# Kernel optimization log

Measured on AMD Instinct MI355X. Metric: run time of the kernel, lower is better.

## Reference

```python
import jax, jax.numpy as jnp
import numpy as np

EMB = 384
GROUPS = 4
B, T = 32, 1024
MAX_DUR = 8
SILENCE_VAL = -11.5129251


def setup_inputs() -> dict:
    key = jax.random.key(0)
    k1, k2, k3, k4, k5 = jax.random.split(key, 5)
    phoneme = jax.random.normal(k1, (B, T, EMB), dtype=jnp.float32)
    durations = jax.random.randint(k2, (B, T + 1), 0, MAX_DUR, dtype=jnp.int32)
    t_out = int(np.asarray(jnp.sum(durations, axis=-1)).max())
    silence_token = jnp.full((EMB,), SILENCE_VAL, dtype=jnp.float32)
    # DurationPredictor params (grouped conv -> ReLU -> 1x1 conv to scalar)
    conv1_w = jax.random.normal(k3, (EMB, EMB // GROUPS, 3), dtype=jnp.float32) * 0.05
    conv1_b = jnp.zeros((EMB,), dtype=jnp.float32)
    conv2_w = jax.random.normal(k4, (1, EMB, 1), dtype=jnp.float32) * 0.05
    conv2_b = jnp.zeros((1,), dtype=jnp.float32)
    return {
        "phoneme": phoneme,
        "silence_token": silence_token,
        "conv1_w": conv1_w,
        "conv1_b": conv1_b,
        "conv2_w": conv2_w,
        "conv2_b": conv2_b,
        "durations": durations,
        "t_out": t_out,
    }


def _duration_predictor(x, conv1_w, conv1_b, conv2_w, conv2_b):
    # x: [B, Tp, E] -> durations_pred [B, Tp]
    xc = jnp.transpose(x, (0, 2, 1))  # [B, E, Tp]
    h = jax.lax.conv_general_dilated(
        xc, conv1_w, window_strides=(1,), padding=((1, 1),),
        dimension_numbers=("NCH", "OIH", "NCH"), feature_group_count=GROUPS)
    h = jax.nn.relu(h + conv1_b[None, :, None])
    d = jax.lax.conv_general_dilated(
        h, conv2_w, window_strides=(1,), padding=((0, 0),),
        dimension_numbers=("NCH", "OIH", "NCH"))
    return d[:, 0, :] + conv2_b[0]  # [B, Tp]


def _regulate(phoneme, durations, t_out):
    # Equivalent to the one-hot mask matmul: frame t gets token j where
    # cumsum[j-1] <= t < cumsum[j]; frames past total length are zero.
    cum = jnp.cumsum(durations, axis=-1)  # [B, Tp]
    pos = jnp.arange(t_out, dtype=cum.dtype)  # [t_out]
    idx = jax.vmap(lambda c: jnp.searchsorted(c, pos, side="right"))(cum)  # [B, t_out]
    valid = pos[None, :] < cum[:, -1:]
    idx = jnp.clip(idx, 0, phoneme.shape[1] - 1)
    gathered = jnp.take_along_axis(phoneme, idx[..., None], axis=1)  # [B, t_out, E]
    return jnp.where(valid[..., None], gathered, jnp.zeros((), phoneme.dtype))


def reference(phoneme, silence_token, conv1_w, conv1_b, conv2_w, conv2_b, durations, t_out):
    Bn = phoneme.shape[0]
    silence = jnp.broadcast_to(silence_token[None, None, :], (Bn, 1, phoneme.shape[2]))
    ph = jnp.concatenate((phoneme, silence), axis=1)  # [B, T+1, E]
    durations_pred = _duration_predictor(ph, conv1_w, conv1_b, conv2_w, conv2_b)
    expanded = _regulate(ph, durations, t_out)  # [B, t_out, E]
    return expanded, durations_pred
```

## Files before the change

### kernel.cpp

```cpp
#include <hip/hip_runtime.h>

#define BATCH 32
#define T_IN 1024
#define TP 1025
#define EMB 384
#define GROUPS 4
#define GC 96
#define KDIM 288

typedef __attribute__((ext_vector_type(8))) short short8;
typedef __attribute__((ext_vector_type(4))) float f32x4;

#define N_WPACK (GROUPS * 9 * 6 * 64 * 8)

__device__ __forceinline__ unsigned short f2bf(float f) {
    union { float f; unsigned u; } v; v.f = f;
    unsigned u = v.u + 0x7fffu + ((v.u >> 16) & 1u);
    return (unsigned short)(u >> 16);
}

__global__ __launch_bounds__(256) void prep_kernel(const float* __restrict__ w1,
                                                   const float* __restrict__ b2,
                                                   unsigned short* __restrict__ wpack,
                                                   float* __restrict__ pred) {
    int i = blockIdx.x * 256 + threadIdx.x;
    if (i < N_WPACK) {
        int j = i & 7;
        int lane = (i >> 3) & 63;
        int rest = i >> 9;
        int nt = rest % 6; rest /= 6;
        int ks = rest % 9;
        int g = rest / 9;
        int oc = nt * 16 + (lane & 15);
        int kk = ks * 32 + (lane >> 4) * 8 + j;
        int k = kk / 96, ic = kk % 96;
        float v = w1[((size_t)(g * GC + oc) * GC + ic) * 3 + k];
        wpack[i] = f2bf(v);
    }
    if (i < BATCH * TP) pred[i] = b2[0];
}

__global__ __launch_bounds__(64) void scan_kernel(const int* __restrict__ dur,
                                                  int* __restrict__ cum) {
    const int b = blockIdx.x;
    const int l = threadIdx.x;
    const int* d = dur + b * TP;
    int* c = cum + b * TP;
    int offset = 0;
    for (int r = 0; r < 17; ++r) {
        int idx = r * 64 + l;
        int v = (idx < TP) ? d[idx] : 0;
        int s = v;
#pragma unroll
        for (int off = 1; off < 64; off <<= 1) {
            int n = __shfl_up(s, off, 64);
            if (l >= off) s += n;
        }
        if (idx < TP) c[idx] = s + offset;
        offset += __shfl(s, 63, 64);
    }
}

__global__ __launch_bounds__(256) void conv_mfma_kernel(const float* __restrict__ phoneme,
                                                        const float* __restrict__ silence,
                                                        const float* __restrict__ b1,
                                                        const float* __restrict__ w2,
                                                        const unsigned short* __restrict__ wpack,
                                                        float* __restrict__ pred) {
    const int tile = blockIdx.x;
    const int g = blockIdx.y;
    const int b = blockIdx.z;
    const int t0 = tile * 64;

    __shared__ __align__(16) unsigned short xs[66][104];
    __shared__ float red[4][16][17];

    const int tid = threadIdx.x;

    for (int e = tid; e < 66 * 24; e += 256) {
        int row = e / 24;
        int v = e - row * 24;
        int r = t0 - 1 + row;
        float4 val;
        if (r < 0 || r > T_IN) {
            val = make_float4(0.f, 0.f, 0.f, 0.f);
        } else if (r == T_IN) {
            val = *(const float4*)(silence + g * GC + v * 4);
        } else {
            val = *(const float4*)(phoneme + ((size_t)(b * T_IN + r)) * EMB + g * GC + v * 4);
        }
        ushort4 pk;
        pk.x = f2bf(val.x); pk.y = f2bf(val.y); pk.z = f2bf(val.z); pk.w = f2bf(val.w);
        *(ushort4*)&xs[row][v * 4] = pk;
    }
    __syncthreads();

    const int w = tid >> 6;
    const int lane = tid & 63;
    const int quad = lane >> 4;
    const int lr = lane & 15;

    f32x4 acc[6];
#pragma unroll
    for (int nt = 0; nt < 6; ++nt) acc[nt] = (f32x4){0.f, 0.f, 0.f, 0.f};

    const unsigned short* wg = wpack + (size_t)g * 9 * 6 * 512;

#pragma unroll
    for (int ks = 0; ks < 9; ++ks) {
        const int k = ks / 3;
        const int icoff = 32 * (ks % 3) + quad * 8;
        const int lrow = w * 16 + lr + k;
        short8 a = *(const short8*)&xs[lrow][icoff];
#pragma unroll
        for (int nt = 0; nt < 6; ++nt) {
            short8 bf = *(const short8*)(wg + ((size_t)(ks * 6 + nt) * 64 + lane) * 8);
            acc[nt] = __builtin_amdgcn_mfma_f32_16x16x32_bf16(a, bf, acc[nt], 0, 0, 0);
        }
    }

    float s[4] = {0.f, 0.f, 0.f, 0.f};
#pragma unroll
    for (int nt = 0; nt < 6; ++nt) {
        int oc = g * GC + nt * 16 + lr;
        float bias = b1[oc];
        float wc = w2[oc];
#pragma unroll
        for (int reg = 0; reg < 4; ++reg) {
            float h = acc[nt][reg] + bias;
            h = h > 0.f ? h : 0.f;
            s[reg] += wc * h;
        }
    }
#pragma unroll
    for (int reg = 0; reg < 4; ++reg) red[w][quad * 4 + reg][lr] = s[reg];
    __syncthreads();

    if (tid < 64) {
        int wv = tid >> 4, m = tid & 15;
        float sum = 0.f;
#pragma unroll
        for (int c2 = 0; c2 < 16; ++c2) sum += red[wv][m][c2];
        int t = t0 + wv * 16 + m;
        if (t < TP) atomicAdd(pred + b * TP + t, sum);
    }
}

__global__ __launch_bounds__(256) void gather_kernel(const float* __restrict__ phoneme,
                                                     const float* __restrict__ silence,
                                                     const int* __restrict__ cum,
                                                     float* __restrict__ out,
                                                     int t_out) {
    const int b = blockIdx.y;
    const int f0 = blockIdx.x * 64;
    const int tid = threadIdx.x;

    __shared__ int sidx[64];
    __shared__ int stotal;

    if (tid == 0) stotal = cum[b * TP + T_IN];
    if (tid < 64) {
        int t = f0 + tid;
        int id = 0;
        if (t < t_out) {
            const int* c = cum + b * TP;
            int lo = 0, hi = TP;
            while (lo < hi) {
                int mid = (lo + hi) >> 1;
                if (c[mid] <= t) lo = mid + 1; else hi = mid;
            }
            id = lo > T_IN ? T_IN : lo;
        }
        sidx[tid] = id;
    }
    __syncthreads();

    const int total = stotal;
    const float4* ph4 = (const float4*)phoneme;
    const float4* s4 = (const float4*)silence;
    float4* out4 = (float4*)out;

    for (int e = tid; e < 64 * 96; e += 256) {
        int fl = e / 96;
        int v = e - fl * 96;
        int t = f0 + fl;
        if (t >= t_out) continue;
        float4 val;
        if (t >= total) {
            val = make_float4(0.f, 0.f, 0.f, 0.f);
        } else {
            int id = sidx[fl];
            val = (id == T_IN) ? s4[v] : ph4[((size_t)(b * T_IN) + id) * 96 + v];
        }
        out4[((size_t)b * t_out + t) * 96 + v] = val;
    }
}

extern "C" void kernel_launch(void* const* d_in, const int* in_sizes, int n_in,
                              void* d_out, int out_size, void* d_ws, size_t ws_size,
                              hipStream_t stream) {
    const float* phoneme = (const float*)d_in[0];
    const float* silence = (const float*)d_in[1];
    const float* conv1_w = (const float*)d_in[2];
    const float* conv1_b = (const float*)d_in[3];
    const float* conv2_w = (const float*)d_in[4];
    const float* conv2_b = (const float*)d_in[5];
    const int* durations = (const int*)d_in[6];
    const int t_out = (out_size - BATCH * TP) / (BATCH * EMB);

    float* out_expanded = (float*)d_out;
    float* out_pred = (float*)d_out + (size_t)BATCH * t_out * EMB;

    int* cum = (int*)d_ws;
    unsigned short* wpack = (unsigned short*)((char*)d_ws + 131200);

    prep_kernel<<<(N_WPACK + 255) / 256, 256, 0, stream>>>(conv1_w, conv2_b, wpack, out_pred);
    scan_kernel<<<BATCH, 64, 0, stream>>>(durations, cum);
    conv_mfma_kernel<<<dim3(17, GROUPS, BATCH), 256, 0, stream>>>(
        phoneme, silence, conv1_b, conv2_w, wpack, out_pred);
    gather_kernel<<<dim3((t_out + 63) / 64, BATCH), 256, 0, stream>>>(
        phoneme, silence, cum, out_expanded, t_out);
}
```

Before: 263.5 us.

## Merge conv groups per block, scatter frame indices, flatten gather

The conv kernel now loads all 384 channels for a 64-frame tile once and assigns one wave per group. Each wave computes four 16-row M tiles, which removes the cross-group atomicAdd and the separate pred initialisation. The duration scan now scatters per-frame token indices (ushort) into workspace in place of the cumulative sums, so the gather kernel skips its per-frame binary search and becomes a flat elementwise copy. The cost is more LDS and accumulator registers per conv block, fewer conv blocks, and serial per-thread scatter loops.

```diff
diff --git a/kernel.cpp b/kernel.cpp
--- a/kernel.cpp
+++ b/kernel.cpp
@@ -6,7 +6,6 @@
 #define EMB 384
 #define GROUPS 4
 #define GC 96
-#define KDIM 288
 
 typedef __attribute__((ext_vector_type(8))) short short8;
 typedef __attribute__((ext_vector_type(4))) float f32x4;
@@ -20,74 +19,83 @@
 }
 
 __global__ __launch_bounds__(256) void prep_kernel(const float* __restrict__ w1,
-                                                   const float* __restrict__ b2,
-                                                   unsigned short* __restrict__ wpack,
-                                                   float* __restrict__ pred) {
+                                                   unsigned short* __restrict__ wpack) {
     int i = blockIdx.x * 256 + threadIdx.x;
-    if (i < N_WPACK) {
-        int j = i & 7;
-        int lane = (i >> 3) & 63;
-        int rest = i >> 9;
-        int nt = rest % 6; rest /= 6;
-        int ks = rest % 9;
-        int g = rest / 9;
-        int oc = nt * 16 + (lane & 15);
-        int kk = ks * 32 + (lane >> 4) * 8 + j;
-        int k = kk / 96, ic = kk % 96;
-        float v = w1[((size_t)(g * GC + oc) * GC + ic) * 3 + k];
-        wpack[i] = f2bf(v);
-    }
-    if (i < BATCH * TP) pred[i] = b2[0];
-}
-
-__global__ __launch_bounds__(64) void scan_kernel(const int* __restrict__ dur,
-                                                  int* __restrict__ cum) {
+    if (i >= N_WPACK) return;
+    int j = i & 7;
+    int lane = (i >> 3) & 63;
+    int rest = i >> 9;
+    int nt = rest % 6; rest /= 6;
+    int ks = rest % 9;
+    int g = rest / 9;
+    int oc = nt * 16 + (lane & 15);
+    int kk = ks * 32 + (lane >> 4) * 8 + j;
+    int k = kk / 96, ic = kk % 96;
+    wpack[i] = f2bf(w1[((size_t)(g * GC + oc) * GC + ic) * 3 + k]);
+}
+
+__global__ __launch_bounds__(256) void scan_scatter_kernel(const int* __restrict__ dur,
+                                                           unsigned short* __restrict__ idx,
+                                                           int t_out) {
     const int b = blockIdx.x;
-    const int l = threadIdx.x;
-    const int* d = dur + b * TP;
-    int* c = cum + b * TP;
-    int offset = 0;
-    for (int r = 0; r < 17; ++r) {
-        int idx = r * 64 + l;
-        int v = (idx < TP) ? d[idx] : 0;
-        int s = v;
-#pragma unroll
-        for (int off = 1; off < 64; off <<= 1) {
-            int n = __shfl_up(s, off, 64);
-            if (l >= off) s += n;
+    const int tid = threadIdx.x;
+    __shared__ int scum[TP];
+
+    if (tid < 64) {
+        const int* d = dur + b * TP;
+        int offset = 0;
+        for (int r = 0; r < 17; ++r) {
+            int i2 = r * 64 + tid;
+            int v = (i2 < TP) ? d[i2] : 0;
+            int s = v;
+#pragma unroll
+            for (int off = 1; off < 64; off <<= 1) {
+                int n = __shfl_up(s, off, 64);
+                if (tid >= off) s += n;
+            }
+            if (i2 < TP) scum[i2] = s + offset;
+            offset += __shfl(s, 63, 64);
         }
-        if (idx < TP) c[idx] = s + offset;
-        offset += __shfl(s, 63, 64);
-    }
+    }
+    __syncthreads();
+
+    unsigned short* ib = idx + (size_t)b * t_out;
+    for (int j = tid; j < TP; j += 256) {
+        int c = scum[j];
+        int d = dur[b * TP + j];
+        for (int f = c - d; f < c; ++f) ib[f] = (unsigned short)j;
+    }
+    const int total = scum[TP - 1];
+    for (int t = total + tid; t < t_out; t += 256) ib[t] = 0xFFFFu;
 }
 
 __global__ __launch_bounds__(256) void conv_mfma_kernel(const float* __restrict__ phoneme,
                                                         const float* __restrict__ silence,
                                                         const float* __restrict__ b1,
                                                         const float* __restrict__ w2,
+                                                        const float* __restrict__ b2,
                                                         const unsigned short* __restrict__ wpack,
                                                         float* __restrict__ pred) {
     const int tile = blockIdx.x;
-    const int g = blockIdx.y;
-    const int b = blockIdx.z;
+    const int b = blockIdx.y;
     const int t0 = tile * 64;
 
-    __shared__ __align__(16) unsigned short xs[66][104];
-    __shared__ float red[4][16][17];
+    __shared__ __align__(16) unsigned short xs[66][392];
+    __shared__ float red[4][64];
 
     const int tid = threadIdx.x;
 
-    for (int e = tid; e < 66 * 24; e += 256) {
-        int row = e / 24;
-        int v = e - row * 24;
+    for (int e = tid; e < 66 * 96; e += 256) {
+        int row = e / 96;
+        int v = e - row * 96;
         int r = t0 - 1 + row;
         float4 val;
         if (r < 0 || r > T_IN) {
             val = make_float4(0.f, 0.f, 0.f, 0.f);
         } else if (r == T_IN) {
-            val = *(const float4*)(silence + g * GC + v * 4);
+            val = *(const float4*)(silence + v * 4);
         } else {
-            val = *(const float4*)(phoneme + ((size_t)(b * T_IN + r)) * EMB + g * GC + v * 4);
+            val = *(const float4*)(phoneme + ((size_t)(b * T_IN + r)) * EMB + v * 4);
         }
         ushort4 pk;
         pk.x = f2bf(val.x); pk.y = f2bf(val.y); pk.z = f2bf(val.z); pk.w = f2bf(val.w);
@@ -95,105 +103,97 @@
     }
     __syncthreads();
 
-    const int w = tid >> 6;
+    const int g = tid >> 6;
     const int lane = tid & 63;
     const int quad = lane >> 4;
     const int lr = lane & 15;
 
-    f32x4 acc[6];
-#pragma unroll
-    for (int nt = 0; nt < 6; ++nt) acc[nt] = (f32x4){0.f, 0.f, 0.f, 0.f};
+    f32x4 acc[4][6];
+#pragma unroll
+    for (int mt = 0; mt < 4; ++mt)
+#pragma unroll
+        for (int nt = 0; nt < 6; ++nt) acc[mt][nt] = (f32x4){0.f, 0.f, 0.f, 0.f};
 
     const unsigned short* wg = wpack + (size_t)g * 9 * 6 * 512;
 
 #pragma unroll
     for (int ks = 0; ks < 9; ++ks) {
-        const int k = ks / 3;
-        const int icoff = 32 * (ks % 3) + quad * 8;
-        const int lrow = w * 16 + lr + k;
-        short8 a = *(const short8*)&xs[lrow][icoff];
+        const int tap = ks / 3;
+        const int col = g * GC + 32 * (ks % 3) + quad * 8;
+        short8 a[4];
+#pragma unroll
+        for (int mt = 0; mt < 4; ++mt)
+            a[mt] = *(const short8*)&xs[mt * 16 + lr + tap][col];
 #pragma unroll
         for (int nt = 0; nt < 6; ++nt) {
             short8 bf = *(const short8*)(wg + ((size_t)(ks * 6 + nt) * 64 + lane) * 8);
-            acc[nt] = __builtin_amdgcn_mfma_f32_16x16x32_bf16(a, bf, acc[nt], 0, 0, 0);
+#pragma unroll
+            for (int mt = 0; mt < 4; ++mt)
+                acc[mt][nt] = __builtin_amdgcn_mfma_f32_16x16x32_bf16(a[mt], bf, acc[mt][nt], 0, 0, 0);
         }
     }
 
-    float s[4] = {0.f, 0.f, 0.f, 0.f};
+    float s[4][4];
+#pragma unroll
+    for (int mt = 0; mt < 4; ++mt)
+#pragma unroll
+        for (int reg = 0; reg < 4; ++reg) s[mt][reg] = 0.f;
 #pragma unroll
     for (int nt = 0; nt < 6; ++nt) {
         int oc = g * GC + nt * 16 + lr;
         float bias = b1[oc];
         float wc = w2[oc];
 #pragma unroll
-        for (int reg = 0; reg < 4; ++reg) {
-            float h = acc[nt][reg] + bias;
-            h = h > 0.f ? h : 0.f;
-            s[reg] += wc * h;
-        }
-    }
-#pragma unroll
-    for (int reg = 0; reg < 4; ++reg) red[w][quad * 4 + reg][lr] = s[reg];
+        for (int mt = 0; mt < 4; ++mt)
+#pragma unroll
+            for (int reg = 0; reg < 4; ++reg) {
+                float h = acc[mt][nt][reg] + bias;
+                h = h > 0.f ? h : 0.f;
+                s[mt][reg] += wc * h;
+            }
+    }
+#pragma unroll
+    for (int off = 1; off < 16; off <<= 1)
+#pragma unroll
+        for (int mt = 0; mt < 4; ++mt)
+#pragma unroll
+            for (int reg = 0; reg < 4; ++reg)
+                s[mt][reg] += __shfl_xor(s[mt][reg], off, 64);
+#pragma unroll
+    for (int mt = 0; mt < 4; ++mt)
+#pragma unroll
+        for (int reg = 0; reg < 4; ++reg)
+            if (lr == mt * 4 + reg) red[g][mt * 16 + quad * 4 + reg] = s[mt][reg];
     __syncthreads();
 
     if (tid < 64) {
-        int wv = tid >> 4, m = tid & 15;
-        float sum = 0.f;
-#pragma unroll
-        for (int c2 = 0; c2 < 16; ++c2) sum += red[wv][m][c2];
-        int t = t0 + wv * 16 + m;
-        if (t < TP) atomicAdd(pred + b * TP + t, sum);
+        int t = t0 + tid;
+        if (t < TP)
+            pred[b * TP + t] = red[0][tid] + red[1][tid] + red[2][tid] + red[3][tid] + b2[0];
     }
 }
 
 __global__ __launch_bounds__(256) void gather_kernel(const float* __restrict__ phoneme,
                                                      const float* __restrict__ silence,
-                                                     const int* __restrict__ cum,
+                                                     const unsigned short* __restrict__ idx,
                                                      float* __restrict__ out,
                                                      int t_out) {
     const int b = blockIdx.y;
-    const int f0 = blockIdx.x * 64;
-    const int tid = threadIdx.x;
-
-    __shared__ int sidx[64];
-    __shared__ int stotal;
-
-    if (tid == 0) stotal = cum[b * TP + T_IN];
-    if (tid < 64) {
-        int t = f0 + tid;
-        int id = 0;
-        if (t < t_out) {
-            const int* c = cum + b * TP;
-            int lo = 0, hi = TP;
-            while (lo < hi) {
-                int mid = (lo + hi) >> 1;
-                if (c[mid] <= t) lo = mid + 1; else hi = mid;
-            }
-            id = lo > T_IN ? T_IN : lo;
-        }
-        sidx[tid] = id;
-    }
-    __syncthreads();
-
-    const int total = stotal;
-    const float4* ph4 = (const float4*)phoneme;
-    const float4* s4 = (const float4*)silence;
-    float4* out4 = (float4*)out;
-
-    for (int e = tid; e < 64 * 96; e += 256) {
-        int fl = e / 96;
-        int v = e - fl * 96;
-        int t = f0 + fl;
-        if (t >= t_out) continue;
-        float4 val;
-        if (t >= total) {
-            val = make_float4(0.f, 0.f, 0.f, 0.f);
-        } else {
-            int id = sidx[fl];
-            val = (id == T_IN) ? s4[v] : ph4[((size_t)(b * T_IN) + id) * 96 + v];
-        }
-        out4[((size_t)b * t_out + t) * 96 + v] = val;
-    }
+    const int nfe = t_out * 96;
+    int e = blockIdx.x * 256 + threadIdx.x;
+    if (e >= nfe) return;
+    int fl = e / 96;
+    int v = e - fl * 96;
+    unsigned short id = idx[(size_t)b * t_out + fl];
+    float4 val;
+    if (id == 0xFFFFu) {
+        val = make_float4(0.f, 0.f, 0.f, 0.f);
+    } else if (id == T_IN) {
+        val = ((const float4*)silence)[v];
+    } else {
+        val = ((const float4*)phoneme)[((size_t)b * T_IN + id) * 96 + v];
+    }
+    ((float4*)out)[(size_t)b * nfe + e] = val;
 }
 
 extern "C" void kernel_launch(void* const* d_in, const int* in_sizes, int n_in,
@@ -211,13 +211,14 @@
     float* out_expanded = (float*)d_out;
     float* out_pred = (float*)d_out + (size_t)BATCH * t_out * EMB;
 
-    int* cum = (int*)d_ws;
-    unsigned short* wpack = (unsigned short*)((char*)d_ws + 131200);
-
-    prep_kernel<<<(N_WPACK + 255) / 256, 256, 0, stream>>>(conv1_w, conv2_b, wpack, out_pred);
-    scan_kernel<<<BATCH, 64, 0, stream>>>(durations, cum);
-    conv_mfma_kernel<<<dim3(17, GROUPS, BATCH), 256, 0, stream>>>(
-        phoneme, silence, conv1_b, conv2_w, wpack, out_pred);
-    gather_kernel<<<dim3((t_out + 63) / 64, BATCH), 256, 0, stream>>>(
-        phoneme, silence, cum, out_expanded, t_out);
-}
+    unsigned short* idx = (unsigned short*)d_ws;
+    size_t idx_bytes = ((size_t)BATCH * t_out * sizeof(unsigned short) + 255) & ~(size_t)255;
+    unsigned short* wpack = (unsigned short*)((char*)d_ws + idx_bytes);
+
+    prep_kernel<<<(N_WPACK + 255) / 256, 256, 0, stream>>>(conv1_w, wpack);
+    scan_scatter_kernel<<<BATCH, 256, 0, stream>>>(durations, idx, t_out);
+    conv_mfma_kernel<<<dim3(17, BATCH), 256, 0, stream>>>(
+        phoneme, silence, conv1_b, conv2_w, conv2_b, wpack, out_pred);
+    gather_kernel<<<dim3((t_out * 96 + 255) / 256, BATCH), 256, 0, stream>>>(
+        phoneme, silence, idx, out_expanded, t_out);
+}
```

Result: slower. 275.0 us (+4.4%).
